# Kernel tuning notes

Hardware: AMD Instinct MI355X
Metric: run time of the kernel (lower is better)

Reference implementation:

```python
import jax, jax.numpy as jnp
import numpy as np

K_SIM_SCHEDULE = [4, 8, 16]
K_CON_SCHEDULE = [2, 4, 8]
NEG = 1000000000.0


def _dual_adjacency(h, k_sim, k_con):
    """Binary causal dual adjacency (similar / dissimilar), no gradient."""
    B, T, D = h.shape
    h = jax.lax.stop_gradient(h)
    xn = h / jnp.maximum(jnp.linalg.norm(h, axis=-1, keepdims=True), 1e-12)
    sim = jnp.einsum('btd,bsd->bts', xn, xn)                 # (B,T,T)
    past = jnp.tril(jnp.ones((T, T), h.dtype), -1)           # strictly-past mask
    sim = sim * past - NEG * (1.0 - past)
    eff_sim = min(k_sim, T - 1)
    eff_con = min(k_con, max(0, T - 1 - eff_sim))
    bI = jnp.arange(B)[:, None, None]
    tI = jnp.arange(T)[None, :, None]
    A_sim = jnp.zeros((B, T, T), h.dtype)
    if eff_sim > 0:
        _, top_idx = jax.lax.top_k(sim, eff_sim)             # (B,T,k)
        A_sim = A_sim.at[bI, tI, top_idx].set(1.0) * past
    A_con = jnp.zeros((B, T, T), h.dtype)
    if eff_con > 0:
        sim_con = jnp.where(A_sim > 0, NEG, sim)
        _, bot_idx = jax.lax.top_k(-sim_con, eff_con)        # smallest eff_con
        A_con = A_con.at[bI, tI, bot_idx].set(1.0) * past * (1.0 - A_sim)
    return A_sim, A_con


def _aggregate(h, A):
    # unweighted mean over selected neighbors; empty rows -> zeros
    deg = jnp.sum(A, axis=-1, keepdims=True)
    return jnp.einsum('bts,bsd->btd', A, h) / jnp.maximum(deg, 1.0)


def setup_inputs() -> dict:
    key = jax.random.key(0)
    ks = jax.random.split(key, 2)
    B, T, D, R = 4, 2048, 512, 3
    x = jax.random.normal(ks[0], (B, T, D), dtype=jnp.float32)
    gain = jnp.ones((R, D), dtype=jnp.float32)
    bias = jnp.zeros((R, D), dtype=jnp.float32)
    log_mix = jnp.zeros((R,), dtype=jnp.float32)
    log_alpha = jnp.zeros((R,), dtype=jnp.float32)
    log_momentum = jnp.asarray(1.0, dtype=jnp.float32)
    log_scale = jnp.asarray(0.0, dtype=jnp.float32)
    return {"x": x, "gain": gain, "bias": bias, "log_mix": log_mix,
            "log_alpha": log_alpha, "log_momentum": log_momentum,
            "log_scale": log_scale}


def reference(x, gain, bias, log_mix, log_alpha, log_momentum, log_scale):
    momentum = jax.nn.sigmoid(log_momentum)
    scale = jax.nn.softplus(log_scale) + 0.01
    h = x
    for r in range(len(K_SIM_SCHEDULE)):
        mix = jax.nn.sigmoid(log_mix[r])
        alpha = jax.nn.sigmoid(log_alpha[r])
        A_sim, A_con = _dual_adjacency(h, K_SIM_SCHEDULE[r], K_CON_SCHEDULE[r])
        msg_pos = _aggregate(h, A_sim)
        msg_neg = _aggregate(h, A_con)
        ctx = alpha * msg_pos + (1.0 - alpha) * msg_neg
        blended = mix * h + (1.0 - mix) * ctx
        h_new = jax.nn.gelu(blended * gain[r] + bias[r], approximate=False)
        h = momentum * h + (1.0 - momentum) * h_new
    return (h - x) * scale
```

## Files before the change

kernel.cpp:

```cpp
#include <hip/hip_runtime.h>
#include <hip/hip_bf16.h>
#include <cstdint>
#include <cstddef>

#define BB 4
#define TT 2048
#define DD 512
#define NEG_INF (-3.402823466e+38f)
#define POS_INF (3.402823466e+38f)

typedef __attribute__((ext_vector_type(8))) short bf16x8;
typedef __attribute__((ext_vector_type(8))) unsigned short ushort8;
typedef __attribute__((ext_vector_type(4))) float f32x4;

__device__ __forceinline__ float sigmoidf_(float x){ return 1.0f/(1.0f+expf(-x)); }

__device__ __forceinline__ unsigned short f2bf(float x){
  __hip_bfloat16 b = __float2bfloat16(x);
  return *reinterpret_cast<unsigned short*>(&b);
}

__device__ __forceinline__ unsigned int fwd_map(float f){
  unsigned int b = __float_as_uint(f);
  return b ^ ((b & 0x80000000u) ? 0xFFFFFFFFu : 0x80000000u);
}
__device__ __forceinline__ float inv_map(unsigned int u){
  unsigned int b = (u & 0x80000000u) ? (u ^ 0x80000000u) : ~u;
  return __uint_as_float(b);
}

__device__ __forceinline__ unsigned long long shfl_xor64(unsigned long long x, int off){
  unsigned int hi = __shfl_xor((unsigned int)(x >> 32), off);
  unsigned int lo = __shfl_xor((unsigned int)x, off);
  return ((unsigned long long)hi << 32) | lo;
}

__global__ __launch_bounds__(64) void k_normsplit(const float* __restrict__ h, float* __restrict__ rnorm,
                                                  unsigned short* __restrict__ Xh, unsigned short* __restrict__ Xl){
  int row = blockIdx.x;
  const float* hr = h + (size_t)row*DD;
  int lane = threadIdx.x;
  float4 v0 = *(const float4*)&hr[lane*4];
  float4 v1 = *(const float4*)&hr[lane*4 + 256];
  float ss = v0.x*v0.x+v0.y*v0.y+v0.z*v0.z+v0.w*v0.w
           + v1.x*v1.x+v1.y*v1.y+v1.z*v1.z+v1.w*v1.w;
  #pragma unroll
  for (int off=32; off; off>>=1) ss += __shfl_xor(ss, off);
  float rn = 1.0f / fmaxf(sqrtf(ss), 1e-12f);
  if (lane==0) rnorm[row] = rn;

  float xs[8] = {v0.x,v0.y,v0.z,v0.w,v1.x,v1.y,v1.z,v1.w};
  unsigned short hb[8], lb[8];
  #pragma unroll
  for (int q=0;q<8;q++){
    float xn = xs[q]*rn;
    unsigned short hh = f2bf(xn);
    __hip_bfloat16 bh = *reinterpret_cast<__hip_bfloat16*>(&hh);
    float rem = xn - __bfloat162float(bh);
    hb[q] = hh; lb[q] = f2bf(rem);
  }
  ushort4 h0 = {hb[0],hb[1],hb[2],hb[3]}, h1 = {hb[4],hb[5],hb[6],hb[7]};
  ushort4 l0 = {lb[0],lb[1],lb[2],lb[3]}, l1 = {lb[4],lb[5],lb[6],lb[7]};
  *(ushort4*)&Xh[(size_t)row*DD + lane*4]       = h0;
  *(ushort4*)&Xh[(size_t)row*DD + lane*4 + 256] = h1;
  *(ushort4*)&Xl[(size_t)row*DD + lane*4]       = l0;
  *(ushort4*)&Xl[(size_t)row*DD + lane*4 + 256] = l1;
}

__global__ __launch_bounds__(256) void k_sim(const unsigned short* __restrict__ Xh,
                                             const unsigned short* __restrict__ Xl,
                                             float* __restrict__ sim,
                                             unsigned short* __restrict__ keys, int b0){
  int p = blockIdx.x;
  int jt = (int)((sqrtf(8.0f*(float)p + 1.0f) - 1.0f)*0.5f);
  while ((jt+1)*(jt+2)/2 <= p) jt++;
  while (jt*(jt+1)/2 > p) jt--;
  int is = p - jt*(jt+1)/2;

  int bl = blockIdx.y;
  size_t xoff = (size_t)(b0 + bl)*TT*DD;
  const unsigned short* XhB = Xh + xoff;
  const unsigned short* XlB = Xl + xoff;
  float* simb = sim + (size_t)bl*TT*TT;
  unsigned short* keyb = keys + (size_t)bl*TT*TT;
  int t0 = jt*128, s0 = is*128;

  __shared__ __align__(16) short As[128*32];
  __shared__ __align__(16) short Bs[128*32];

  int tid = threadIdx.x, wave = tid>>6, lane = tid&63;
  int wr = wave>>1, wc = wave&1;

  int srow = tid>>2;
  int sc8  = (tid&3)*8;

  f32x4 acc[4][4];
  #pragma unroll
  for (int m=0;m<4;m++)
    #pragma unroll
    for (int n=0;n<4;n++) acc[m][n] = (f32x4){0.f,0.f,0.f,0.f};

  ushort8 ra0, ra1, rb0, rb1;
  auto gload = [&](int s){
    int pass = s>>4; int kcol = (s&15)*32;
    const unsigned short* sA = (pass<2) ? XhB : XlB;
    const unsigned short* sB = (pass!=1) ? XhB : XlB;
    ra0 = *(const ushort8*)&sA[(size_t)(t0+srow)*DD + kcol + sc8];
    ra1 = *(const ushort8*)&sA[(size_t)(t0+srow+64)*DD + kcol + sc8];
    rb0 = *(const ushort8*)&sB[(size_t)(s0+srow)*DD + kcol + sc8];
    rb1 = *(const ushort8*)&sB[(size_t)(s0+srow+64)*DD + kcol + sc8];
  };

  gload(0);
  for (int s=0; s<48; ++s){
    __syncthreads();
    *(ushort8*)&As[srow*32 + sc8]      = ra0;
    *(ushort8*)&As[(srow+64)*32 + sc8] = ra1;
    *(ushort8*)&Bs[srow*32 + sc8]      = rb0;
    *(ushort8*)&Bs[(srow+64)*32 + sc8] = rb1;
    __syncthreads();
    if (s < 47) gload(s+1);

    int arow = wr*64 + (lane&15);
    int brow = wc*64 + (lane&15);
    int kb = (lane>>4)*8;
    bf16x8 af[4], bf[4];
    #pragma unroll
    for (int m=0;m<4;m++) af[m] = *(const bf16x8*)&As[(arow + m*16)*32 + kb];
    #pragma unroll
    for (int n=0;n<4;n++) bf[n] = *(const bf16x8*)&Bs[(brow + n*16)*32 + kb];
    #pragma unroll
    for (int m=0;m<4;m++)
      #pragma unroll
      for (int n=0;n<4;n++)
        acc[m][n] = __builtin_amdgcn_mfma_f32_16x16x32_bf16(af[m], bf[n], acc[m][n], 0, 0, 0);
  }

  #pragma unroll
  for (int m=0;m<4;m++){
    int t = t0 + wr*64 + m*16 + (lane>>4)*4;
    #pragma unroll
    for (int n=0;n<4;n++){
      int sc = s0 + wc*64 + n*16 + (lane&15);
      float* dst = simb + (size_t)t*TT + sc;
      unsigned short* kdst = keyb + (size_t)t*TT + sc;
      #pragma unroll
      for (int j=0;j<4;j++){
        float v = acc[m][n][j];
        dst[(size_t)j*TT] = v;
        kdst[(size_t)j*TT] = (unsigned short)(fwd_map(v) >> 16);
      }
    }
  }
}

#define BMASK 0xFFFFFF00u

#define KLO(D,S) ( ((D) << 16)         | (0x7FFu - (unsigned int)(S)) )
#define KHI(D,S) ( ((D) & 0xFFFF0000u) | (0x7FFu - (unsigned int)(S)) )
#define INS32(KK) do{ unsigned int a=(KK); \
  if (a > kv3){ unsigned int q=kv3; if (q > cert) cert = q; \
    if (a > kv0){ q=kv0; kv0=a; a=q; } \
    if (a > kv1){ q=kv1; kv1=a; a=q; } \
    if (a > kv2){ q=kv2; kv2=a; a=q; } \
    kv3=a; } \
  else { if (a > cert) cert = a; } }while(0)
#define PROC8(W,S) { INS32(KLO((W).x,(S)));   INS32(KHI((W).x,(S)+1)); \
                     INS32(KLO((W).y,(S)+2)); INS32(KHI((W).y,(S)+3)); \
                     INS32(KLO((W).z,(S)+4)); INS32(KHI((W).z,(S)+5)); \
                     INS32(KLO((W).w,(S)+6)); INS32(KHI((W).w,(S)+7)); }

__device__ __forceinline__ unsigned int radix24(const float* __restrict__ srow, int t, int k1,
                                                unsigned int flip, int* sh, int lane){
  #pragma unroll
  for (int i=0;i<4;i++) sh[lane + i*64] = 0;
  int t4 = t & ~3;
  for (int s4 = lane*4; s4 < t4; s4 += 256){
    float4 f = *(const float4*)&srow[s4];
    unsigned int u0=fwd_map(f.x)^flip, u1=fwd_map(f.y)^flip, u2=fwd_map(f.z)^flip, u3=fwd_map(f.w)^flip;
    atomicAdd(&sh[u0>>24],1); atomicAdd(&sh[u1>>24],1);
    atomicAdd(&sh[u2>>24],1); atomicAdd(&sh[u3>>24],1);
  }
  for (int s = t4 + lane; s < t; s += 64){
    unsigned int u = fwd_map(srow[s])^flip;
    atomicAdd(&sh[u>>24],1);
  }
  unsigned int pfx = 0u; int kp = k1;
  #pragma unroll
  for (int pass = 0; pass < 3; ++pass){
    int shift = 24 - 8*pass;
    int m4 = sh[4*lane] + sh[4*lane+1] + sh[4*lane+2] + sh[4*lane+3];
    int x = __shfl(m4, 63-lane);
    #pragma unroll
    for (int off = 1; off < 64; off <<= 1){
      int v = __shfl_up(x, off);
      if (lane >= off) x += v;
    }
    int T = __shfl(x, 63-lane);
    int G = T - m4;
    bool hit = (G < kp) && (kp <= T);
    unsigned int npfx = 0u; int nkp = 0;
    if (hit){
      int c = G; int D = 4*lane;
      #pragma unroll
      for (int i = 3; i >= 0; --i){
        int hc = sh[4*lane + i];
        if (kp <= c + hc){ D = 4*lane + i; break; }
        c += hc;
      }
      npfx = pfx | ((unsigned int)D << shift);
      nkp = kp - c;
    }
    unsigned long long hm = __ballot(hit);
    int src = __ffsll(hm) - 1;
    pfx = __shfl(npfx, src);
    kp  = __shfl(nkp, src);
    if (pass == 2) break;

    int nshift = shift - 8;
    unsigned int keep = 0xFFFFFFFFu << shift;
    #pragma unroll
    for (int i=0;i<4;i++) sh[lane + i*64] = 0;
    for (int s4 = lane*4; s4 < t4; s4 += 256){
      float4 f = *(const float4*)&srow[s4];
      unsigned int u0=fwd_map(f.x)^flip, u1=fwd_map(f.y)^flip, u2=fwd_map(f.z)^flip, u3=fwd_map(f.w)^flip;
      if (((u0 ^ pfx) & keep) == 0) atomicAdd(&sh[(u0>>nshift)&255],1);
      if (((u1 ^ pfx) & keep) == 0) atomicAdd(&sh[(u1>>nshift)&255],1);
      if (((u2 ^ pfx) & keep) == 0) atomicAdd(&sh[(u2>>nshift)&255],1);
      if (((u3 ^ pfx) & keep) == 0) atomicAdd(&sh[(u3>>nshift)&255],1);
    }
    for (int s = t4 + lane; s < t; s += 64){
      unsigned int u = fwd_map(srow[s])^flip;
      if (((u ^ pfx) & keep) == 0) atomicAdd(&sh[(u>>nshift)&255],1);
    }
  }
  return pfx;
}

template<int ESIM, int ECON>
__global__ __launch_bounds__(256) void k_topk(const float* __restrict__ sim,
                                              const unsigned short* __restrict__ keys, int b0,
                                              const float* __restrict__ h, const float* __restrict__ rnorm,
                                              int* __restrict__ topidx, int* __restrict__ botidx,
                                              int* __restrict__ bcnt){
  constexpr int K1  = ESIM + 8;
  constexpr int K1B = ESIM + ECON + 8;
  constexpr int CANDCAP = 44;
  constexpr int EQCAP = 44;
  constexpr float TAU = 5e-5f;
  __shared__ int s_hist[4][256];
  __shared__ int s_cand[4][CANDCAP];
  __shared__ int s_eq[4][EQCAP];
  __shared__ int s_sel[4][ESIM];
  __shared__ int s_bot[4][16];
  __shared__ int s_cnt[4][2];

  int tid = threadIdx.x, lane = tid & 63, wid = tid >> 6;
  int lrow = blockIdx.x*4 + wid;
  int bl = lrow >> 11, t = lrow & (TT-1);
  int gb = b0 + bl;
  int grow = (gb << 11) | t;

  if (t <= ESIM){
    if (lane < t) topidx[(size_t)grow*16 + lane] = lane;
    if (lane == 0) bcnt[grow] = 0;
    return;
  }
  const float* srow = sim + (size_t)lrow*TT;
  const unsigned short* krow = keys + (size_t)lrow*TT;
  const float* hb  = h + (size_t)gb*TT*DD;
  const float* rnb = rnorm + (size_t)gb*TT;

  int* sh    = s_hist[wid];
  int* scand = s_cand[wid];
  int* seq   = s_eq[wid];
  int* ssel  = s_sel[wid];
  int* sbot  = s_bot[wid];
  int t4 = t & ~3;
  unsigned long long below = (lane == 0) ? 0ull : ((~0ull) >> (64 - lane));

  unsigned int kv0=0, kv1=0, kv2=0, kv3=0, cert=0;
  {
    int nd  = t >> 1;
    int nd4 = nd >> 2;
    const uint4* kr4 = (const uint4*)krow;
    uint4 w0, w1, w2, w3;
    bool g0 = (lane       < nd4);
    bool g1 = (lane +  64 < nd4);
    bool g2 = (lane + 128 < nd4);
    bool g3 = (lane + 192 < nd4);
    if (g0) w0 = kr4[lane];
    if (g1) w1 = kr4[lane + 64];
    if (g2) w2 = kr4[lane + 128];
    if (g3) w3 = kr4[lane + 192];
    if (g0) PROC8(w0, (lane)*8);
    if (g1) PROC8(w1, (lane+64)*8);
    if (g2) PROC8(w2, (lane+128)*8);
    if (g3) PROC8(w3, (lane+192)*8);
    for (int d = nd4*4 + lane; d < nd; d += 64){
      unsigned int w = ((const unsigned int*)krow)[d];
      int s = 2*d;
      INS32(KLO(w, s)); INS32(KHI(w, s+1));
    }
    if ((t & 1) && lane == 0){
      unsigned int u16 = krow[t-1];
      INS32((u16 << 16) | (0x7FFu - (unsigned int)(t-1)));
    }
  }

  int ck = (kv0?1:0) + (kv1?1:0) + (kv2?1:0) + (kv3?1:0);
  unsigned long long kb0=__ballot(ck&1), kb1=__ballot(ck&2), kb2=__ballot(ck&4);
  int kept = __popcll(kb0) + 2*__popcll(kb1) + 4*__popcll(kb2);
  int ncand = min(min(t, K1), kept);

  bool fb = false, done = false;
  if (ncand > ESIM){
    unsigned int v = 0;
    for (int bit = 31; bit >= 0; --bit){
      unsigned int test = v | (1u << bit);
      int c = (kv0>=test) + (kv1>=test) + (kv2>=test) + (kv3>=test);
      unsigned long long c0=__ballot(c&1), c1=__ballot(c&2), c2=__ballot(c&4);
      int cnt = __popcll(c0) + 2*__popcll(c1) + 4*__popcll(c2);
      if (cnt >= ncand) v = test;
    }
    unsigned int m = 0;
    if (kv0 < v) m = kv0;
    else if (kv1 < v) m = kv1;
    else if (kv2 < v) m = kv2;
    else if (kv3 < v) m = kv3;
    unsigned int mo = (cert > m) ? cert : m;
    #pragma unroll
    for (int off=32; off; off>>=1){
      unsigned int om = __shfl_xor(mo, off);
      if (om > mo) mo = om;
    }
    unsigned int b_out16 = mo >> 16;

    int ci = (kv0>=v) + (kv1>=v) + (kv2>=v) + (kv3>=v);
    unsigned long long p0=__ballot(ci&1), p1=__ballot(ci&2), p2=__ballot(ci&4);
    int pre = __popcll(p0&below) + 2*__popcll(p1&below) + 4*__popcll(p2&below);
    if (ci > 0) scand[pre]   = (int)kv0;
    if (ci > 1) scand[pre+1] = (int)kv1;
    if (ci > 2) scand[pre+2] = (int)kv2;
    if (ci > 3) scand[pre+3] = (int)kv3;

    unsigned int pk = (lane < ncand) ? (unsigned int)scand[lane] : 0u;
    unsigned int npk = ~pk;
    #pragma unroll
    for (int kk = 2; kk <= 32; kk <<= 1){
      #pragma unroll
      for (int j = kk >> 1; j > 0; j >>= 1){
        unsigned int o = __shfl_xor(npk, j);
        bool keepMin = (((lane & kk) == 0) == ((lane & j) == 0));
        bool less = (npk < o);
        npk = (keepMin == less) ? npk : o;
      }
    }
    pk = ~npk;

    unsigned int pA = __shfl(pk, ESIM-1);
    unsigned int pB = __shfl(pk, ESIM);
    unsigned int bA = pA >> 16, bB = pB >> 16;
    unsigned int M  = (bB > b_out16) ? bB : b_out16;

    bool t1 = false;
    if (bA > M && M < 0xFFFFu){
      float loA = inv_map(bA << 16);
      float hiM = inv_map((M + 1) << 16);
      t1 = (loA - hiM >= TAU);
    }
    if (t1){
      if (lane < ESIM){
        int idx = 0x7FF - (int)(pk & 0xFFFFu);
        ssel[lane] = idx;
        topidx[(size_t)grow*16 + lane] = idx;
      }
      done = true;
    } else {
      unsigned int thc = bB;
      int cnt = 0;
      int nd = t >> 1;
      const unsigned int* kd = (const unsigned int*)krow;
      for (int d0 = 0; d0 < nd; d0 += 64){
        int d = d0 + lane;
        bool in = (d < nd);
        unsigned int w = in ? kd[d] : 0u;
        bool e0 = in && ((w & 0xFFFFu) >= thc);
        bool e1 = in && ((w >> 16)     >= thc);
        unsigned long long m0 = __ballot(e0), m1 = __ballot(e1);
        int n0 = __popcll(m0);
        int bpos0 = cnt + __popcll(m0 & below);
        int bpos1 = cnt + n0 + __popcll(m1 & below);
        if (e0 && bpos0 < CANDCAP) scand[bpos0] = 2*d;
        if (e1 && bpos1 < CANDCAP) scand[bpos1] = 2*d + 1;
        cnt += n0 + __popcll(m1);
      }
      if (t & 1){
        unsigned int kk16 = krow[t-1];
        if (kk16 >= thc){
          if (lane == 0 && cnt < CANDCAP) scand[cnt] = t-1;
          cnt++;
        }
      }
      if (cnt > CANDCAP){
        fb = true;
      } else {
        int nc = cnt;
        unsigned long long key = 0ull;
        if (lane < nc){
          int idx = scand[lane];
          float f = srow[idx];
          key = (((unsigned long long)fwd_map(f)) << 32) | (unsigned int)(~idx);
        }
        unsigned long long nk = ~key;
        #pragma unroll
        for (int kk = 2; kk <= 64; kk <<= 1){
          #pragma unroll
          for (int j = kk >> 1; j > 0; j >>= 1){
            unsigned long long o = shfl_xor64(nk, j);
            bool keepMin = (((lane & kk) == 0) == ((lane & j) == 0));
            bool less = (nk < o);
            nk = (keepMin == less) ? nk : o;
          }
        }
        key = ~nk;
        int   idx_l = (int)(~(unsigned int)key);
        float val   = inv_map((unsigned int)(key >> 32));
        float vA = __shfl(val, ESIM-1);
        float vB = __shfl(val, ESIM);
        if (vA - vB < TAU){
          fb = true;
        } else {
          if (lane < ESIM){
            ssel[lane] = idx_l;
            topidx[(size_t)grow*16 + lane] = idx_l;
          }
          done = true;
        }
      }
    }
  } else {
    fb = true;
  }

  if (fb){
    int k1 = min(t, K1);
    unsigned int thr = radix24(srow, t, k1, 0u, sh, lane);

    if (lane == 0){ s_cnt[wid][0] = 0; s_cnt[wid][1] = 0; }
    for (int s4 = lane*4; s4 < t4; s4 += 256){
      float4 f = *(const float4*)&srow[s4];
      unsigned int uu[4] = {fwd_map(f.x), fwd_map(f.y), fwd_map(f.z), fwd_map(f.w)};
      #pragma unroll
      for (int q=0;q<4;q++){
        unsigned int b24 = uu[q] & BMASK;
        if (b24 > thr){ int p = atomicAdd(&s_cnt[wid][0],1); if (p < CANDCAP) scand[p] = s4+q; }
        else if (b24 == thr){ int p = atomicAdd(&s_cnt[wid][1],1); if (p < EQCAP) seq[p] = s4+q; }
      }
    }
    for (int s = t4 + lane; s < t; s += 64){
      unsigned int b24 = fwd_map(srow[s]) & BMASK;
      if (b24 > thr){ int p = atomicAdd(&s_cnt[wid][0],1); if (p < CANDCAP) scand[p] = s; }
      else if (b24 == thr){ int p = atomicAdd(&s_cnt[wid][1],1); if (p < EQCAP) seq[p] = s; }
    }
    int c_gt = min(s_cnt[wid][0], CANDCAP);
    int c_eq = min(s_cnt[wid][1], EQCAP);
    int ncand2 = min(c_gt + c_eq, 64);

    unsigned int myu = 0u; int myi = 0x7fffffff;
    if (lane < ncand2){
      myi = (lane < c_gt) ? scand[lane] : seq[lane - c_gt];
      myu = fwd_map(srow[myi]);
    }

    float fvA = 0.f, fvB = 0.f;
    {
      unsigned int cu = myu; int ci2 = myi;
      #pragma unroll
      for (int k = 0; k <= ESIM; ++k){
        unsigned int bu = cu; int bi = ci2;
        #pragma unroll
        for (int off=32; off; off>>=1){
          unsigned int ou = __shfl_xor(bu, off); int oi = __shfl_xor(bi, off);
          if (ou > bu || (ou == bu && oi < bi)){ bu = ou; bi = oi; }
        }
        if (k < ESIM && lane == 0) ssel[k] = bi;
        if (k == ESIM-1) fvA = inv_map(bu);
        if (k == ESIM)   fvB = inv_map(bu);
        if (ci2 == bi){ cu = 0u; ci2 = 0x7fffffff; }
      }
    }

    bool resc = (fvA - fvB < TAU);
    if (resc){
      const float* hq = hb + (size_t)t*DD;
      float rt = rnb[t];
      float4 qq0 = *(const float4*)&hq[lane*4];
      float4 qq1 = *(const float4*)&hq[lane*4 + 256];
      float ev = NEG_INF;
      for (int j = 0; j < ncand2; ++j){
        int idx = (j < c_gt) ? scand[j] : seq[j - c_gt];
        const float* hc = hb + (size_t)idx*DD;
        float4 c0 = *(const float4*)&hc[lane*4];
        float4 c1 = *(const float4*)&hc[lane*4 + 256];
        float pp = qq0.x*c0.x+qq0.y*c0.y+qq0.z*c0.z+qq0.w*c0.w
                 + qq1.x*c1.x+qq1.y*c1.y+qq1.z*c1.z+qq1.w*c1.w;
        #pragma unroll
        for (int off=32; off; off>>=1) pp += __shfl_xor(pp, off);
        float ex = pp * rt * rnb[idx];
        if (lane == j) ev = ex;
      }
      float rv = (lane < ncand2) ? ev : NEG_INF;
      int   ri = myi;
      #pragma unroll
      for (int k = 0; k < ESIM; ++k){
        float bv = rv; int bi = ri;
        #pragma unroll
        for (int off=32; off; off>>=1){
          float ov = __shfl_xor(bv, off); int oi = __shfl_xor(bi, off);
          if (ov > bv || (ov == bv && oi < bi)){ bv = ov; bi = oi; }
        }
        if (lane == 0) ssel[k] = bi;
        if (ri == bi) rv = NEG_INF;
      }
    }
    if (lane < ESIM) topidx[(size_t)grow*16 + lane] = ssel[lane];
  }

  int need = ECON - (TT - t);
  int cnt2 = 0;
  if (need > 0){
    constexpr unsigned int FLIP = 0xFFFFFFFFu;
    int k1b = min(t, K1B);
    unsigned int thrb = radix24(srow, t, k1b, FLIP, sh, lane);

    if (lane == 0){ s_cnt[wid][0] = 0; s_cnt[wid][1] = 0; }
    for (int s4 = lane*4; s4 < t4; s4 += 256){
      float4 f = *(const float4*)&srow[s4];
      unsigned int uu[4] = {fwd_map(f.x)^FLIP, fwd_map(f.y)^FLIP, fwd_map(f.z)^FLIP, fwd_map(f.w)^FLIP};
      #pragma unroll
      for (int q=0;q<4;q++){
        unsigned int b24 = uu[q] & BMASK;
        if (b24 > thrb){ int p = atomicAdd(&s_cnt[wid][0],1); if (p < CANDCAP) scand[p] = s4+q; }
        else if (b24 == thrb){ int p = atomicAdd(&s_cnt[wid][1],1); if (p < EQCAP) seq[p] = s4+q; }
      }
    }
    for (int s = t4 + lane; s < t; s += 64){
      unsigned int u = fwd_map(srow[s])^FLIP;
      unsigned int b24 = u & BMASK;
      if (b24 > thrb){ int p = atomicAdd(&s_cnt[wid][0],1); if (p < CANDCAP) scand[p] = s; }
      else if (b24 == thrb){ int p = atomicAdd(&s_cnt[wid][1],1); if (p < EQCAP) seq[p] = s; }
    }
    int bc_gt = min(s_cnt[wid][0], CANDCAP);
    int bc_eq = min(s_cnt[wid][1], EQCAP);
    int ncb = min(bc_gt + bc_eq, 64);

    unsigned int mu = 0u; int mi = 0x7fffffff;
    if (lane < ncb){
      mi = (lane < bc_gt) ? scand[lane] : seq[lane - bc_gt];
      mu = fwd_map(srow[mi]) ^ FLIP;
    }
    float wA = 0.f, wB = 0.f;
    unsigned int cu = mu; int ci3 = mi;
    #pragma unroll
    for (int k = 0; k < K1B; ++k){
      if (k < ncb && cnt2 < need + 8){
        unsigned int bu = cu; int bi = ci3;
        #pragma unroll
        for (int off=32; off; off>>=1){
          unsigned int ou = __shfl_xor(bu, off); int oi = __shfl_xor(bi, off);
          if (ou > bu || (ou == bu && oi < bi)){ bu = ou; bi = oi; }
        }
        if (ci3 == bi){ cu = 0u; ci3 = 0x7fffffff; }
        bool mem = false;
        #pragma unroll
        for (int j=0;j<ESIM;j++) if (ssel[j] == bi) mem = true;
        if (!mem){
          if (lane == 0) sbot[cnt2] = bi;
          float val = inv_map(bu ^ FLIP);
          if (cnt2 == need-1) wA = val;
          if (cnt2 == need)   wB = val;
          cnt2++;
        }
      }
    }
    int npick = min(need, cnt2);
    bool rb = (cnt2 > need) && (wB - wA < TAU);
    if (!rb){
      if (lane < npick) botidx[(size_t)grow*8 + lane] = sbot[lane];
    } else {
      const float* hq = hb + (size_t)t*DD;
      float rt = rnb[t];
      float4 qq0 = *(const float4*)&hq[lane*4];
      float4 qq1 = *(const float4*)&hq[lane*4 + 256];
      float ev = POS_INF; int ei = 0x7fffffff;
      for (int j = 0; j < cnt2; ++j){
        int idx = sbot[j];
        const float* hc = hb + (size_t)idx*DD;
        float4 c0 = *(const float4*)&hc[lane*4];
        float4 c1 = *(const float4*)&hc[lane*4 + 256];
        float pp = qq0.x*c0.x+qq0.y*c0.y+qq0.z*c0.z+qq0.w*c0.w
                 + qq1.x*c1.x+qq1.y*c1.y+qq1.z*c1.z+qq1.w*c1.w;
        #pragma unroll
        for (int off=32; off; off>>=1) pp += __shfl_xor(pp, off);
        float ex = pp * rt * rnb[idx];
        if (lane == j){ ev = ex; ei = idx; }
      }
      #pragma unroll
      for (int k = 0; k < ECON; ++k){
        if (k < npick){
          float bv = ev; int bi = ei;
          #pragma unroll
          for (int off=32; off; off>>=1){
            float ov = __shfl_xor(bv, off); int oi = __shfl_xor(bi, off);
            if (ov < bv || (ov == bv && oi < bi)){ bv = ov; bi = oi; }
          }
          if (lane == 0) botidx[(size_t)grow*8 + k] = bi;
          if (ei == bi) ev = POS_INF;
        }
      }
    }
    cnt2 = npick;
  }
  if (lane == 0) bcnt[grow] = cnt2;
}

__global__ __launch_bounds__(256) void k_agg(const float* __restrict__ hsrc, float* __restrict__ hdst,
                                             const int* __restrict__ topidx, const int* __restrict__ botidx,
                                             const int* __restrict__ bcnt,
                                             const float* __restrict__ gain, const float* __restrict__ bias,
                                             const float* __restrict__ log_mix, const float* __restrict__ log_alpha,
                                             const float* __restrict__ log_momentum, int r, int eff_sim){
  int row = blockIdx.x;
  int b = row >> 11; int t = row & (TT-1);
  int n_sim = min(eff_sim, t);
  int n_con = bcnt[row];
  float mix      = sigmoidf_(log_mix[r]);
  float alpha    = sigmoidf_(log_alpha[r]);
  float momentum = sigmoidf_(log_momentum[0]);
  const float* hb = hsrc + (size_t)b*TT*DD;

  __shared__ int sidx[16];
  __shared__ int scidx[8];
  if (threadIdx.x < 16) sidx[threadIdx.x]  = (threadIdx.x < n_sim) ? topidx[(size_t)row*16 + threadIdx.x] : 0;
  if (threadIdx.x < 8)  scidx[threadIdx.x] = (threadIdx.x < n_con) ? botidx[(size_t)row*8  + threadIdx.x] : 0;
  __syncthreads();

  #pragma unroll
  for (int e = threadIdx.x; e < DD; e += 256){
    float sp = 0.f;
    for (int j=0;j<n_sim;j++) sp += hb[(size_t)sidx[j]*DD + e];
    float sn = 0.f;
    for (int j=0;j<n_con;j++) sn += hb[(size_t)scidx[j]*DD + e];
    float mp = sp / (float)max(n_sim, 1);
    float mn = sn / (float)max(n_con, 1);
    float ctx = alpha*mp + (1.f-alpha)*mn;
    float hv = hsrc[(size_t)row*DD + e];
    float blended = mix*hv + (1.f-mix)*ctx;
    float u = blended*gain[e] + bias[e];
    float g = 0.5f*u*(1.0f + erff(u*0.7071067811865475f));
    hdst[(size_t)row*DD + e] = momentum*hv + (1.f-momentum)*g;
  }
}

__global__ __launch_bounds__(256) void k_final(const float* __restrict__ hfin, const float* __restrict__ x,
                                               const float* __restrict__ log_scale, float* __restrict__ out, int n){
  float scale = log1pf(expf(log_scale[0])) + 0.01f;
  int i = blockIdx.x*256 + threadIdx.x;
  if (i < n) out[i] = (hfin[i] - x[i]) * scale;
}

extern "C" void kernel_launch(void* const* d_in, const int* in_sizes, int n_in,
                              void* d_out, int out_size, void* d_ws, size_t ws_size,
                              hipStream_t stream) {
  const float* x         = (const float*)d_in[0];
  const float* gain      = (const float*)d_in[1];
  const float* bias      = (const float*)d_in[2];
  const float* log_mix   = (const float*)d_in[3];
  const float* log_alpha = (const float*)d_in[4];
  const float* log_mom   = (const float*)d_in[5];
  const float* log_scale = (const float*)d_in[6];

  float* hA = (float*)d_out;
  char* ws = (char*)d_ws;
  size_t off = 0;
  auto alloc = [&](size_t bytes){ void* p = ws + off; off += (bytes + 255) & ~(size_t)255; return p; };

  float*          hB     = (float*)alloc((size_t)BB*TT*DD*4);
  float*          rnorm  = (float*)alloc((size_t)BB*TT*4);
  int*            topidx = (int*)  alloc((size_t)BB*TT*16*4);
  int*            botidx = (int*)  alloc((size_t)BB*TT*8*4);
  int*            bcnt   = (int*)  alloc((size_t)BB*TT*4);
  unsigned short* Xh     = (unsigned short*)alloc((size_t)BB*TT*DD*2);
  unsigned short* Xl     = (unsigned short*)alloc((size_t)BB*TT*DD*2);

  size_t rem = (ws_size > off) ? (ws_size - off) : 0;
  int cb = (int)(rem / ((size_t)TT*TT*6 + 512));
  if (cb < 1) cb = 1;
  if (cb > BB) cb = BB;
  float*          sim  = (float*)alloc((size_t)cb*TT*TT*4);
  unsigned short* keys = (unsigned short*)alloc((size_t)cb*TT*TT*2);

  const float* hsrc = x;
  float* hdst = hB;
  const int ks[3] = {4, 8, 16};

  for (int r = 0; r < 3; ++r){
    k_normsplit<<<BB*TT, 64, 0, stream>>>(hsrc, rnorm, Xh, Xl);
    for (int b0 = 0; b0 < BB; b0 += cb){
      int nb = (BB - b0 < cb) ? (BB - b0) : cb;
      dim3 g(136, nb);
      k_sim<<<g, 256, 0, stream>>>(Xh, Xl, sim, keys, b0);
      if (r == 0)      k_topk<4,2><<<nb*TT/4, 256, 0, stream>>>(sim, keys, b0, hsrc, rnorm, topidx, botidx, bcnt);
      else if (r == 1) k_topk<8,4><<<nb*TT/4, 256, 0, stream>>>(sim, keys, b0, hsrc, rnorm, topidx, botidx, bcnt);
      else             k_topk<16,8><<<nb*TT/4, 256, 0, stream>>>(sim, keys, b0, hsrc, rnorm, topidx, botidx, bcnt);
    }
    k_agg<<<BB*TT, 256, 0, stream>>>(hsrc, hdst, topidx, botidx, bcnt,
                                     gain + (size_t)r*DD, bias + (size_t)r*DD,
                                     log_mix, log_alpha, log_mom, r, ks[r]);
    if (r == 0){ hsrc = hB; hdst = hA; }
    else if (r == 1){ hsrc = hA; hdst = hB; }
  }
  k_final<<<(BB*TT*DD)/256, 256, 0, stream>>>(hB, x, log_scale, (float*)d_out, BB*TT*DD);
}
```

Before: 482.1 us.

## Use direct global-to-LDS loads with double buffering and 8 waves in k_sim

```diff
diff --git a/kernel.cpp b/kernel.cpp
--- a/kernel.cpp
+++ b/kernel.cpp
@@ -33,6 +33,12 @@
   unsigned int hi = __shfl_xor((unsigned int)(x >> 32), off);
   unsigned int lo = __shfl_xor((unsigned int)x, off);
   return ((unsigned long long)hi << 32) | lo;
+}
+
+__device__ __forceinline__ void gl_lds16(const unsigned short* g, short* l){
+  __builtin_amdgcn_global_load_lds(
+    (const __attribute__((address_space(1))) unsigned int*)g,
+    (__attribute__((address_space(3))) unsigned int*)l, 16, 0, 0);
 }
 
 __global__ __launch_bounds__(64) void k_normsplit(const float* __restrict__ h, float* __restrict__ rnorm,
@@ -67,7 +73,7 @@
   *(ushort4*)&Xl[(size_t)row*DD + lane*4 + 256] = l1;
 }
 
-__global__ __launch_bounds__(256) void k_sim(const unsigned short* __restrict__ Xh,
+__global__ __launch_bounds__(512) void k_sim(const unsigned short* __restrict__ Xh,
                                              const unsigned short* __restrict__ Xl,
                                              float* __restrict__ sim,
                                              unsigned short* __restrict__ keys, int b0){
@@ -85,63 +91,61 @@
   unsigned short* keyb = keys + (size_t)bl*TT*TT;
   int t0 = jt*128, s0 = is*128;
 
-  __shared__ __align__(16) short As[128*32];
-  __shared__ __align__(16) short Bs[128*32];
+  __shared__ __align__(16) short As[2][4096];
+  __shared__ __align__(16) short Bs[2][4096];
 
   int tid = threadIdx.x, wave = tid>>6, lane = tid&63;
-  int wr = wave>>1, wc = wave&1;
+  int wr = wave>>2, wc = wave&3;
 
   int srow = tid>>2;
   int sc8  = (tid&3)*8;
 
-  f32x4 acc[4][4];
+  size_t offA = (size_t)(t0 + srow)*DD + sc8;
+  size_t offB = (size_t)(s0 + srow)*DD + sc8;
+
+  f32x4 acc[4][2];
   #pragma unroll
   for (int m=0;m<4;m++)
     #pragma unroll
-    for (int n=0;n<4;n++) acc[m][n] = (f32x4){0.f,0.f,0.f,0.f};
-
-  ushort8 ra0, ra1, rb0, rb1;
-  auto gload = [&](int s){
+    for (int n=0;n<2;n++) acc[m][n] = (f32x4){0.f,0.f,0.f,0.f};
+
+  auto stage = [&](int s, int buf){
     int pass = s>>4; int kcol = (s&15)*32;
     const unsigned short* sA = (pass<2) ? XhB : XlB;
     const unsigned short* sB = (pass!=1) ? XhB : XlB;
-    ra0 = *(const ushort8*)&sA[(size_t)(t0+srow)*DD + kcol + sc8];
-    ra1 = *(const ushort8*)&sA[(size_t)(t0+srow+64)*DD + kcol + sc8];
-    rb0 = *(const ushort8*)&sB[(size_t)(s0+srow)*DD + kcol + sc8];
-    rb1 = *(const ushort8*)&sB[(size_t)(s0+srow+64)*DD + kcol + sc8];
+    gl_lds16(sA + offA + kcol, &As[buf][wave*512]);
+    gl_lds16(sB + offB + kcol, &Bs[buf][wave*512]);
   };
 
-  gload(0);
+  stage(0, 0);
+  __syncthreads();
+
+  int arow = wr*64 + (lane&15);
+  int brow = wc*32 + (lane&15);
+  int kb = (lane>>4)*8;
+
   for (int s=0; s<48; ++s){
+    int cur = s & 1;
+    if (s < 47) stage(s+1, cur^1);
+    bf16x8 af[4], bf[2];
+    #pragma unroll
+    for (int m=0;m<4;m++) af[m] = *(const bf16x8*)&As[cur][(arow + m*16)*32 + kb];
+    #pragma unroll
+    for (int n=0;n<2;n++) bf[n] = *(const bf16x8*)&Bs[cur][(brow + n*16)*32 + kb];
+    #pragma unroll
+    for (int m=0;m<4;m++)
+      #pragma unroll
+      for (int n=0;n<2;n++)
+        acc[m][n] = __builtin_amdgcn_mfma_f32_16x16x32_bf16(af[m], bf[n], acc[m][n], 0, 0, 0);
     __syncthreads();
-    *(ushort8*)&As[srow*32 + sc8]      = ra0;
-    *(ushort8*)&As[(srow+64)*32 + sc8] = ra1;
-    *(ushort8*)&Bs[srow*32 + sc8]      = rb0;
-    *(ushort8*)&Bs[(srow+64)*32 + sc8] = rb1;
-    __syncthreads();
-    if (s < 47) gload(s+1);
-
-    int arow = wr*64 + (lane&15);
-    int brow = wc*64 + (lane&15);
-    int kb = (lane>>4)*8;
-    bf16x8 af[4], bf[4];
-    #pragma unroll
-    for (int m=0;m<4;m++) af[m] = *(const bf16x8*)&As[(arow + m*16)*32 + kb];
-    #pragma unroll
-    for (int n=0;n<4;n++) bf[n] = *(const bf16x8*)&Bs[(brow + n*16)*32 + kb];
-    #pragma unroll
-    for (int m=0;m<4;m++)
-      #pragma unroll
-      for (int n=0;n<4;n++)
-        acc[m][n] = __builtin_amdgcn_mfma_f32_16x16x32_bf16(af[m], bf[n], acc[m][n], 0, 0, 0);
   }
 
   #pragma unroll
   for (int m=0;m<4;m++){
     int t = t0 + wr*64 + m*16 + (lane>>4)*4;
     #pragma unroll
-    for (int n=0;n<4;n++){
-      int sc = s0 + wc*64 + n*16 + (lane&15);
+    for (int n=0;n<2;n++){
+      int sc = s0 + wc*32 + n*16 + (lane&15);
       float* dst = simb + (size_t)t*TT + sc;
       unsigned short* kdst = keyb + (size_t)t*TT + sc;
       #pragma unroll
@@ -313,7 +317,7 @@
   int kept = __popcll(kb0) + 2*__popcll(kb1) + 4*__popcll(kb2);
   int ncand = min(min(t, K1), kept);
 
-  bool fb = false, done = false;
+  bool fb = false;
   if (ncand > ESIM){
     unsigned int v = 0;
     for (int bit = 31; bit >= 0; --bit){
@@ -375,7 +379,6 @@
         ssel[lane] = idx;
         topidx[(size_t)grow*16 + lane] = idx;
       }
-      done = true;
     } else {
       unsigned int thc = bB;
       int cnt = 0;
@@ -435,7 +438,6 @@
             ssel[lane] = idx_l;
             topidx[(size_t)grow*16 + lane] = idx_l;
           }
-          done = true;
         }
       }
     }
@@ -710,7 +712,7 @@
     for (int b0 = 0; b0 < BB; b0 += cb){
       int nb = (BB - b0 < cb) ? (BB - b0) : cb;
       dim3 g(136, nb);
-      k_sim<<<g, 256, 0, stream>>>(Xh, Xl, sim, keys, b0);
+      k_sim<<<g, 512, 0, stream>>>(Xh, Xl, sim, keys, b0);
       if (r == 0)      k_topk<4,2><<<nb*TT/4, 256, 0, stream>>>(sim, keys, b0, hsrc, rnorm, topidx, botidx, bcnt);
       else if (r == 1) k_topk<8,4><<<nb*TT/4, 256, 0, stream>>>(sim, keys, b0, hsrc, rnorm, topidx, botidx, bcnt);
       else             k_topk<16,8><<<nb*TT/4, 256, 0, stream>>>(sim, keys, b0, hsrc, rnorm, topidx, botidx, bcnt);
```

Measured after the change: 476.5 us. No clear change (-1.2%).
